# Kernel optimization log

Hardware: AMD Instinct MI355X
Metric: run time of the kernel (lower is better)

The kernel has to match this reference:

```python
import jax, jax.numpy as jnp
import numpy as np

# ---- problem sizes ----
N_CELLS = 128
V_PER = 64            # vertices per cell
F_PER = 124           # faces per cell (2V-4 for closed sphere-like mesh)
N_V = N_CELLS * V_PER # 8192
N_F = N_CELLS * F_PER # 15872

# ---- module hyperparameters (init kwargs) ----
N_ITERS = 5
TIME_STEP = 1e-5
THRESH = 0.3
P_RANGE = (10.0, 200.0)
ST_RANGE = (0.002, 0.02)
TARGET_VOL = 1.0
BULK = 2500.0
UF_ITERS = 8          # label-propagation rounds for union-find


def setup_inputs() -> dict:
    rng = np.random.default_rng(0)
    # cell centers on an 8x4x4 grid, spacing 0.8 so radius-0.5 spheres overlap
    centers = np.stack(np.meshgrid(np.arange(8), np.arange(4), np.arange(4), indexing='ij'), -1)
    centers = centers.reshape(-1, 3).astype(np.float32) * 0.8
    d = rng.normal(size=(N_CELLS, V_PER, 3)).astype(np.float32)
    d /= (np.linalg.norm(d, axis=-1, keepdims=True) + 1e-9)
    verts = (centers[:, None, :] + 0.5 * d).reshape(N_V, 3).astype(np.float32)
    local = rng.integers(0, V_PER, size=(N_CELLS, F_PER, 3))
    faces = (local + np.arange(N_CELLS)[:, None, None] * V_PER).reshape(N_F, 3).astype(np.int32)
    face_cell_index = np.repeat(np.arange(N_CELLS), F_PER).astype(np.int32)
    cell_face_list = np.arange(N_F, dtype=np.int32).reshape(N_CELLS, F_PER)
    vertex_cell = np.repeat(np.arange(N_CELLS), V_PER).astype(np.int32)
    vc = verts.reshape(N_CELLS, V_PER, 3)
    bounding_boxes = np.concatenate([vc.min(1), vc.max(1)], axis=-1).astype(np.float32)
    return {
        'vertices': jnp.asarray(verts),
        'bounding_boxes': jnp.asarray(bounding_boxes),
        'normalized_pressure': jnp.float32(0.5),
        'normalized_surface_tension': jnp.float32(0.5),
        'faces': jnp.asarray(faces),
        'face_cell_index': jnp.asarray(face_cell_index),
        'cell_face_list': jnp.asarray(cell_face_list),
        'vertex_cell': jnp.asarray(vertex_cell),
    }


def _union_find(contact):
    # min-label propagation + pointer jumping; components here are tiny clusters
    def body(_, labels):
        nm = jnp.min(jnp.where(contact, labels[None, :], N_V), axis=1)
        labels = jnp.minimum(labels, nm)
        return labels[labels]
    return jax.lax.fori_loop(0, UF_ITERS, body, jnp.arange(N_V, dtype=jnp.int32))


def _group_mean(x, labels):
    s = jax.ops.segment_sum(x, labels, num_segments=N_V)
    c = jax.ops.segment_sum(jnp.ones((x.shape[0],), x.dtype), labels, num_segments=N_V)
    return (s / jnp.maximum(c, 1.0)[:, None])[labels]


def _energy(verts, faces, cell_face_list, surface_tension, target_vol):
    # surface-tension energy: st * total face area
    v0, v1, v2 = verts[faces[:, 0]], verts[faces[:, 1]], verts[faces[:, 2]]
    n = jnp.cross(v1 - v0, v2 - v0)
    areas = 0.5 * jnp.sqrt(jnp.sum(n * n, -1) + 1e-12)
    e_tension = surface_tension * jnp.sum(areas)
    # pressure/volume energy: K/2 * (V_c - V_target)^2, volume wrt cell centroid
    centroids = verts.reshape(N_CELLS, V_PER, 3).mean(axis=1)  # (C,3)
    fv = faces[cell_face_list]                                  # (C,Fc,3)
    p0 = verts[fv[..., 0]] - centroids[:, None, :]
    p1 = verts[fv[..., 1]] - centroids[:, None, :]
    p2 = verts[fv[..., 2]] - centroids[:, None, :]
    vols = jnp.sum(jnp.einsum('cfi,cfi->cf', p0, jnp.cross(p1, p2)), axis=1) / 6.0
    e_vol = 0.5 * BULK * jnp.sum((vols - target_vol) ** 2)
    return e_tension + e_vol


def _forward(vertices, bounding_boxes, normalized_pressure, normalized_surface_tension,
             faces, cell_face_list, vertex_cell):
    pressure = normalized_pressure * (P_RANGE[1] - P_RANGE[0]) + P_RANGE[0]
    surface_tension = normalized_surface_tension * (ST_RANGE[1] - ST_RANGE[0]) + ST_RANGE[0]
    target_vol = TARGET_VOL * jnp.exp(pressure / BULK)
    # pairwise bbox intersection over cells (fixed bboxes, as in the source)
    mins, maxs = bounding_boxes[:, :3], bounding_boxes[:, 3:]
    cell_contact = (jnp.all(mins[:, None] <= maxs[None, :], -1) &
                    jnp.all(mins[None, :] <= maxs[:, None], -1))
    cell_contact = cell_contact & ~jnp.eye(N_CELLS, dtype=bool)
    verts = vertices
    for _ in range(N_ITERS):
        # pairwise vertex distances, gated by cell contact graph
        sq = jnp.sum(verts * verts, -1)
        d2 = sq[:, None] + sq[None, :] - 2.0 * (verts @ verts.T)
        contact = (d2 < THRESH * THRESH) & cell_contact[vertex_cell[:, None], vertex_cell[None, :]]
        labels = _union_find(contact)
        verts = _group_mean(verts, labels)
        forces = -jax.grad(_energy)(verts, faces, cell_face_list, surface_tension, target_vol)
        forces = _group_mean(forces, labels)
        verts = verts + TIME_STEP * forces
    return verts


def reference(vertices, bounding_boxes, normalized_pressure, normalized_surface_tension,
              faces, face_cell_index, cell_face_list, vertex_cell):
    del face_cell_index  # vertex_cell carries the per-vertex cell ids we need
    return _forward(vertices, bounding_boxes, normalized_pressure, normalized_surface_tension,
                    faces, cell_face_list, vertex_cell)
```

## Files before the change

kernel.cpp:

```cpp
#include <hip/hip_runtime.h>

#define NV 8192
#define NC 128
#define VP 64
#define FP 124
#define MAXSLOT 26
#define NSL 7

typedef unsigned long long ull;

__device__ __forceinline__ int findro(const int* parent, int x) {
  int p = parent[x];
  while (p != x) { x = p; p = parent[x]; }
  return x;
}
__device__ __forceinline__ void ghook(int* parent, int a0, int b0) {
  int a = a0, b = b0;
  for (;;) {
    a = findro(parent, a);
    b = findro(parent, b);
    if (a == b) break;
    int hi = a > b ? a : b, lo = a > b ? b : a;
    int old = atomicMin(&parent[hi], lo);
    if (old == hi) { a = lo; b = lo; break; }
    a = old; b = lo;
  }
  int r = a < b ? a : b;
  if (r < a0) atomicMin(&parent[a0], r);
  if (r < b0) atomicMin(&parent[b0], r);
}

__device__ __forceinline__ void recon3(const float* ps1, const float* ps2,
                                       const float* pc, int l,
                                       float& x, float& y, float& z) {
  float cc = fmaxf(pc[l], 1.f);
  x = ps1[3*l+0]/cc + 1e-5f*(ps2[3*l+0]/cc);
  y = ps1[3*l+1]/cc + 1e-5f*(ps2[3*l+1]/cc);
  z = ps1[3*l+2]/cc + 1e-5f*(ps2[3*l+2]/cc);
}

__device__ __forceinline__ int build_adj(const float* bb, int c, int q, int v,
                                         int t, int* s_hcell, ull* s_adjw,
                                         int* s_KH) {
  if (q < 2) {
    int b = q * 64 + v;
    float anx = bb[c*6+0], any_ = bb[c*6+1], anz = bb[c*6+2];
    float axx = bb[c*6+3], axy = bb[c*6+4], axz = bb[c*6+5];
    float bnx = bb[b*6+0], bny = bb[b*6+1], bnz = bb[b*6+2];
    float bxx = bb[b*6+3], bxy = bb[b*6+4], bxz = bb[b*6+5];
    bool ov = (b != c) && (anx <= bxx) && (any_ <= bxy) && (anz <= bxz) &&
              (bnx <= axx) && (bny <= axy) && (bnz <= axz);
    bool mine = ov && (((c + b) & 1) ? (b < c) : (b > c));
    ull w = __ballot(mine);
    if (v == 0) s_adjw[q] = w;
  }
  __syncthreads();
  if (t == 0) {
    int slot = 0;
    for (int wd = 0; wd < 2; ++wd) {
      ull aw = s_adjw[wd];
      while (aw) {
        int bbit = __ffsll((long long)aw) - 1; aw &= aw - 1;
        if (slot < MAXSLOT) s_hcell[slot] = wd * 64 + bbit;
        ++slot;
      }
    }
    *s_KH = slot;
  }
  __syncthreads();
  return *s_KH;
}

__global__ void k_init(int* __restrict__ parent) {
  int i = blockIdx.x * blockDim.x + threadIdx.x;
  if (i < NV) parent[i] = i;
}

__global__ __launch_bounds__(256, 1)
void k_contact(int it, const float* __restrict__ inV, const float* __restrict__ bb,
               const int* __restrict__ labelsF, const float* __restrict__ ps1,
               const float* __restrict__ pc, const float* __restrict__ ps2,
               float* __restrict__ verts, int* __restrict__ llab,
               ull* __restrict__ masks) {
  const float T2 = (float)(0.3 * 0.3);
  const int c = blockIdx.x;
  const int t = threadIdx.x;
  const int q = t >> 6;
  const int v = t & 63;

  __shared__ float s_vx[VP], s_vy[VP], s_vz[VP], s_sq[VP];
  __shared__ int   s_hcell[MAXSLOT];
  __shared__ int   s_KH;
  __shared__ ull   s_adjw[2];
  __shared__ ull   s_Mw[4][VP];

  const int KH = build_adj(bb, c, q, v, t, s_hcell, s_adjw, &s_KH);

  if (t < VP) {
    int i = c*VP + t;
    float x, y, z;
    if (it == 0) { x = inV[3*i+0]; y = inV[3*i+1]; z = inV[3*i+2]; }
    else         { recon3(ps1, ps2, pc, labelsF[i], x, y, z); }
    s_vx[t] = x; s_vy[t] = y; s_vz[t] = z; s_sq[t] = x*x + y*y + z*z;
    verts[3*i+0] = x; verts[3*i+1] = y; verts[3*i+2] = z;
  }
  __syncthreads();

  ull msk[NSL];
  {
    float xs[NSL], ys[NSL], zs[NSL];
#pragma unroll
    for (int s = 0; s < NSL; ++s) {
      msk[s] = 0;
      int slot = q + 4*s;
      if (slot < KH) {
        int jb = s_hcell[slot]*VP;
        if (it == 0) {
          int j = jb + v;
          xs[s] = inV[3*j+0]; ys[s] = inV[3*j+1]; zs[s] = inV[3*j+2];
        } else {
          int lF = labelsF[jb + v];
          recon3(ps1, ps2, pc, lF, xs[s], ys[s], zs[s]);
        }
      }
    }
#pragma unroll
    for (int s = 0; s < NSL; ++s) { int slot = q + 4*s; if (slot < KH) {
      float X = xs[s], Y = ys[s], Z = zs[s];
      float sqj = X*X + Y*Y + Z*Z;
      ull w = 0;
      for (int vv = 0; vv < VP; ++vv) {
        float d2 = s_sq[vv] + sqj - 2.f*(s_vx[vv]*X + s_vy[vv]*Y + s_vz[vv]*Z);
        if (d2 < T2) w |= (1ull << vv);
      }
      msk[s] = w;
      masks[((size_t)c*MAXSLOT + slot)*VP + v] = w;
    } }
  }

  ull M = 1ull << v;
#pragma unroll
  for (int s = 0; s < NSL; ++s) {
    ull any = __ballot(msk[s] != 0);
    if (any) {
#pragma unroll
      for (int k = 0; k < 64; ++k) {
        ull ck = __shfl(msk[s], k);
        if ((ck >> v) & 1) M |= ck;
      }
    }
  }
  s_Mw[q][v] = M;
  __syncthreads();
  M = s_Mw[0][v] | s_Mw[1][v] | s_Mw[2][v] | s_Mw[3][v];
#pragma unroll
  for (int k = 0; k < 64; ++k) {
    ull rk = __shfl(M, k);
    if ((M >> k) & 1) M |= rk;
  }
  if (q == 0) llab[c*VP + v] = c*VP + (__ffsll((long long)M) - 1);
}

__global__ __launch_bounds__(256, 1)
void k_hook(const float* __restrict__ bb, const int* __restrict__ llab,
            const ull* __restrict__ masks, int* __restrict__ parent) {
  const int c = blockIdx.x;
  const int t = threadIdx.x;
  const int q = t >> 6;
  const int v = t & 63;

  __shared__ int s_hcell[MAXSLOT];
  __shared__ int s_KH;
  __shared__ ull s_adjw[2];

  const int KH = build_adj(bb, c, q, v, t, s_hcell, s_adjw, &s_KH);

#pragma unroll
  for (int s = 0; s < NSL; ++s) { int slot = q + 4*s; if (slot < KH) {
    int jb = s_hcell[slot]*VP;
    ull w = masks[((size_t)c*MAXSLOT + slot)*VP + v];
    int L = -1, Lb = -1;
    if (w) {
      L  = llab[c*VP + (__ffsll((long long)w) - 1)];
      Lb = llab[jb + v];
    }
    ull act = __ballot(w != 0);
    while (act) {
      int lead = __ffsll((long long)act) - 1;
      int Ll  = __shfl(L,  lead);
      int Lbl = __shfl(Lb, lead);
      ull grp = __ballot(L == Ll && Lb == Lbl && w != 0) & act;
      if (v == lead) ghook(parent, Ll, Lbl);
      act &= ~grp;
    }
  } }
}

__global__ __launch_bounds__(64, 1)
void k_find(const int* __restrict__ parent, const int* __restrict__ llab,
            int* __restrict__ labelsF, const float* __restrict__ verts,
            float* __restrict__ cs1, float* __restrict__ cc1,
            float* __restrict__ zs1, float* __restrict__ zc,
            float* __restrict__ zs2) {
  const int c = blockIdx.x, t = threadIdx.x;
  __shared__ int   s_lab[VP];
  __shared__ float s_vx[VP], s_vy[VP], s_vz[VP];
  int i = c*VP + t;
  int l = findro(parent, llab[i]);
  s_lab[t] = l;
  labelsF[i] = l;
  s_vx[t] = verts[3*i+0]; s_vy[t] = verts[3*i+1]; s_vz[t] = verts[3*i+2];
  for (int idx = t; idx < VP*3; idx += VP) {
    zs1[c*VP*3 + idx] = 0.f;
    zs2[c*VP*3 + idx] = 0.f;
  }
  zc[i] = 0.f;
  __syncthreads();
  {
    bool leader = true;
    for (int s = 0; s < t; ++s) if (s_lab[s] == l) { leader = false; break; }
    if (leader) {
      float sx = 0.f, sy = 0.f, sz = 0.f, cn = 0.f;
      for (int s = t; s < VP; ++s)
        if (s_lab[s] == l) { sx += s_vx[s]; sy += s_vy[s]; sz += s_vz[s]; cn += 1.f; }
      atomicAdd(&cs1[3*l+0], sx);
      atomicAdd(&cs1[3*l+1], sy);
      atomicAdd(&cs1[3*l+2], sz);
      atomicAdd(&cc1[l], cn);
    }
  }
}

__global__ __launch_bounds__(128, 1)
void k_forces(const int* __restrict__ labelsF, const int* __restrict__ faces,
              const int* __restrict__ cfl, const float* __restrict__ pP,
              const float* __restrict__ pS,
              const float* __restrict__ cs1, const float* __restrict__ cc1,
              float* __restrict__ cs2, int* __restrict__ parent) {
  const int c = blockIdx.x, t = threadIdx.x;
  __shared__ float s_vx[VP], s_vy[VP], s_vz[VP];
  __shared__ float s_gx[VP], s_gy[VP], s_gz[VP];
  __shared__ float s_fx[VP], s_fy[VP], s_fz[VP];
  __shared__ int   s_lab[VP];
  __shared__ float s_cx, s_cy, s_cz, s_vol, s_csx, s_csy, s_csz;

  if (t < VP) {
    int i = c*VP + t;
    int l = labelsF[i];
    s_lab[t] = l;
    float cc = fmaxf(cc1[l], 1.f);
    s_vx[t] = cs1[3*l+0] / cc;
    s_vy[t] = cs1[3*l+1] / cc;
    s_vz[t] = cs1[3*l+2] / cc;
    s_gx[t] = 0.f; s_gy[t] = 0.f; s_gz[t] = 0.f;
    parent[i] = i;
  }
  if (t == 0) { s_vol = 0.f; s_csx = 0.f; s_csy = 0.f; s_csz = 0.f; }
  __syncthreads();
  if (t < VP) {
    float sx = s_vx[t], sy = s_vy[t], sz = s_vz[t];
#pragma unroll
    for (int o = 32; o; o >>= 1) { sx += __shfl_xor(sx, o); sy += __shfl_xor(sy, o); sz += __shfl_xor(sz, o); }
    if (t == 0) { s_cx = sx*(1.f/VP); s_cy = sy*(1.f/VP); s_cz = sz*(1.f/VP); }
  }
  __syncthreads();
  float cx = s_cx, cy = s_cy, cz = s_cz;
  bool act = (t < FP);
  int ia = 0, ib = 0, ic = 0;
  float p0x=0,p0y=0,p0z=0,p1x=0,p1y=0,p1z=0,p2x=0,p2y=0,p2z=0;
  float q0x=0,q0y=0,q0z=0;
  if (act) {
    int f = cfl[c*FP + t];
    ia = faces[3*f+0] - c*VP; ib = faces[3*f+1] - c*VP; ic = faces[3*f+2] - c*VP;
    p0x = s_vx[ia]-cx; p0y = s_vy[ia]-cy; p0z = s_vz[ia]-cz;
    p1x = s_vx[ib]-cx; p1y = s_vy[ib]-cy; p1z = s_vz[ib]-cz;
    p2x = s_vx[ic]-cx; p2y = s_vy[ic]-cy; p2z = s_vz[ic]-cz;
    q0x = p1y*p2z - p1z*p2y;
    q0y = p1z*p2x - p1x*p2z;
    q0z = p1x*p2y - p1y*p2x;
    float term = p0x*q0x + p0y*q0y + p0z*q0z;
    atomicAdd(&s_vol, term);
  }
  __syncthreads();
  float press = pP[0]*190.f + 10.f;
  float st    = pS[0]*0.018f + 0.002f;
  float tv    = expf(press / 2500.f);
  float vol   = s_vol / 6.f;
  float coeff = 2500.f * (vol - tv);
  if (act) {
    float q1x = p2y*p0z - p2z*p0y;
    float q1y = p2z*p0x - p2x*p0z;
    float q1z = p2x*p0y - p2y*p0x;
    float q2x = p0y*p1z - p0z*p1y;
    float q2y = p0z*p1x - p0x*p1z;
    float q2z = p0x*p1y - p0y*p1x;
    float e1x = p1x-p0x, e1y = p1y-p0y, e1z = p1z-p0z;
    float e2x = p2x-p0x, e2y = p2y-p0y, e2z = p2z-p0z;
    float nx = e1y*e2z - e1z*e2y;
    float ny = e1z*e2x - e1x*e2z;
    float nz = e1x*e2y - e1y*e2x;
    float S  = nx*nx + ny*ny + nz*nz + 1e-12f;
    float wt = st / (2.f * sqrtf(S));
    float dx = e1x-e2x, dy = e1y-e2y, dz = e1z-e2z;
    float g0x = wt*(dy*nz - dz*ny), g0y = wt*(dz*nx - dx*nz), g0z = wt*(dx*ny - dy*nx);
    float g1x = wt*(e2y*nz - e2z*ny), g1y = wt*(e2z*nx - e2x*nz), g1z = wt*(e2x*ny - e2y*nx);
    float g2x = wt*(ny*e1z - nz*e1y), g2y = wt*(nz*e1x - nx*e1z), g2z = wt*(nx*e1y - ny*e1x);
    float k = coeff / 6.f;
    atomicAdd(&s_gx[ia], g0x + k*q0x); atomicAdd(&s_gy[ia], g0y + k*q0y); atomicAdd(&s_gz[ia], g0z + k*q0z);
    atomicAdd(&s_gx[ib], g1x + k*q1x); atomicAdd(&s_gy[ib], g1y + k*q1y); atomicAdd(&s_gz[ib], g1z + k*q1z);
    atomicAdd(&s_gx[ic], g2x + k*q2x); atomicAdd(&s_gy[ic], g2y + k*q2y); atomicAdd(&s_gz[ic], g2z + k*q2z);
    atomicAdd(&s_csx, q0x+q1x+q2x);
    atomicAdd(&s_csy, q0y+q1y+q2y);
    atomicAdd(&s_csz, q0z+q1z+q2z);
  }
  __syncthreads();
  if (t < VP) {
    float corr = coeff / 384.f;
    s_fx[t] = -(s_gx[t] - corr*s_csx);
    s_fy[t] = -(s_gy[t] - corr*s_csy);
    s_fz[t] = -(s_gz[t] - corr*s_csz);
  }
  __syncthreads();
  if (t < VP) {
    int l = s_lab[t];
    bool leader = true;
    for (int s = 0; s < t; ++s) if (s_lab[s] == l) { leader = false; break; }
    if (leader) {
      float sx = 0.f, sy = 0.f, sz = 0.f;
      for (int s = t; s < VP; ++s)
        if (s_lab[s] == l) { sx += s_fx[s]; sy += s_fy[s]; sz += s_fz[s]; }
      atomicAdd(&cs2[3*l+0], sx);
      atomicAdd(&cs2[3*l+1], sy);
      atomicAdd(&cs2[3*l+2], sz);
    }
  }
}

__global__ __launch_bounds__(64, 1)
void k_out(const int* __restrict__ labelsF, const float* __restrict__ cs1,
           const float* __restrict__ cc1, const float* __restrict__ cs2,
           float* __restrict__ out) {
  const int c = blockIdx.x, t = threadIdx.x;
  int i = c*VP + t;
  int l = labelsF[i];
  float cc = fmaxf(cc1[l], 1.f);
  out[3*i+0] = cs1[3*l+0]/cc + 1e-5f*(cs2[3*l+0]/cc);
  out[3*i+1] = cs1[3*l+1]/cc + 1e-5f*(cs2[3*l+1]/cc);
  out[3*i+2] = cs1[3*l+2]/cc + 1e-5f*(cs2[3*l+2]/cc);
}

extern "C" void kernel_launch(void* const* d_in, const int* in_sizes, int n_in,
                              void* d_out, int out_size, void* d_ws, size_t ws_size,
                              hipStream_t stream) {
  const float* inV   = (const float*)d_in[0];
  const float* bb    = (const float*)d_in[1];
  const float* pP    = (const float*)d_in[2];
  const float* pS    = (const float*)d_in[3];
  const int*   faces = (const int*)d_in[4];
  const int*   cfl   = (const int*)d_in[6];

  char* w = (char*)d_ws;
  int*   parent  = (int*)w;   w += NV*sizeof(int);
  int*   labelsF = (int*)w;   w += NV*sizeof(int);
  int*   llab    = (int*)w;   w += NV*sizeof(int);
  float* verts   = (float*)w; w += NV*3*sizeof(float);
  float* zbase   = (float*)w;
  float* sumsA   = (float*)w; w += 2*NV*3*sizeof(float);
  float* countsA = (float*)w; w += 2*NV*sizeof(float);
  float* sumsB   = (float*)w; w += 2*NV*3*sizeof(float);
  ull*   masks   = (ull*)w;   w += (size_t)NC*MAXSLOT*VP*sizeof(ull);

  hipMemsetAsync(zbase, 0, (2*NV*3 + 2*NV + 2*NV*3)*sizeof(float), stream);
  k_init<<<NV/256, 256, 0, stream>>>(parent);

  for (int it = 0; it < 5; ++it) {
    const int p = it & 1;
    float* cs1 = sumsA + p*(NV*3);
    float* cc1 = countsA + p*NV;
    float* cs2 = sumsB + p*(NV*3);
    float* ps1 = sumsA + (p^1)*(NV*3);
    float* pc  = countsA + (p^1)*NV;
    float* ps2 = sumsB + (p^1)*(NV*3);

    k_contact<<<NC, 256, 0, stream>>>(it, inV, bb, labelsF, ps1, pc, ps2,
                                      verts, llab, masks);
    k_hook<<<NC, 256, 0, stream>>>(bb, llab, masks, parent);
    k_find<<<NC, 64, 0, stream>>>(parent, llab, labelsF, verts,
                                  cs1, cc1, ps1, pc, ps2);
    k_forces<<<NC, 128, 0, stream>>>(labelsF, faces, cfl, pP, pS,
                                     cs1, cc1, cs2, parent);
  }
  k_out<<<NC, 64, 0, stream>>>(labelsF, sumsA, countsA, sumsB, (float*)d_out);
}
```

Measured before the change: 411.0 us.

## Fuse hook pass into contact kernel, hooking union-find directly from register masks

```diff
diff --git a/kernel.cpp b/kernel.cpp
--- a/kernel.cpp
+++ b/kernel.cpp
@@ -80,8 +80,7 @@
 void k_contact(int it, const float* __restrict__ inV, const float* __restrict__ bb,
                const int* __restrict__ labelsF, const float* __restrict__ ps1,
                const float* __restrict__ pc, const float* __restrict__ ps2,
-               float* __restrict__ verts, int* __restrict__ llab,
-               ull* __restrict__ masks) {
+               float* __restrict__ verts, int* __restrict__ parent) {
   const float T2 = (float)(0.3 * 0.3);
   const int c = blockIdx.x;
   const int t = threadIdx.x;
@@ -91,6 +90,7 @@
   __shared__ float s_vx[VP], s_vy[VP], s_vz[VP], s_sq[VP];
   __shared__ int   s_hcell[MAXSLOT];
   __shared__ int   s_KH;
+  __shared__ int   s_llv[VP];
   __shared__ ull   s_adjw[2];
   __shared__ ull   s_Mw[4][VP];
 
@@ -134,7 +134,6 @@
         if (d2 < T2) w |= (1ull << vv);
       }
       msk[s] = w;
-      masks[((size_t)c*MAXSLOT + slot)*VP + v] = w;
     } }
   }
 
@@ -158,47 +157,37 @@
     ull rk = __shfl(M, k);
     if ((M >> k) & 1) M |= rk;
   }
-  if (q == 0) llab[c*VP + v] = c*VP + (__ffsll((long long)M) - 1);
-}
-
-__global__ __launch_bounds__(256, 1)
-void k_hook(const float* __restrict__ bb, const int* __restrict__ llab,
-            const ull* __restrict__ masks, int* __restrict__ parent) {
-  const int c = blockIdx.x;
-  const int t = threadIdx.x;
-  const int q = t >> 6;
-  const int v = t & 63;
-
-  __shared__ int s_hcell[MAXSLOT];
-  __shared__ int s_KH;
-  __shared__ ull s_adjw[2];
-
-  const int KH = build_adj(bb, c, q, v, t, s_hcell, s_adjw, &s_KH);
+  const int ll = __ffsll((long long)M) - 1;
+  if (q == 0) s_llv[v] = ll;
+  __syncthreads();
+
+  if (q == 0 && ll != v) ghook(parent, c*VP + v, c*VP + ll);
 
 #pragma unroll
   for (int s = 0; s < NSL; ++s) { int slot = q + 4*s; if (slot < KH) {
     int jb = s_hcell[slot]*VP;
-    ull w = masks[((size_t)c*MAXSLOT + slot)*VP + v];
-    int L = -1, Lb = -1;
-    if (w) {
-      L  = llab[c*VP + (__ffsll((long long)w) - 1)];
-      Lb = llab[jb + v];
-    }
+    ull w = msk[s];
+    int L = -1;
+    if (w) L = s_llv[__ffsll((long long)w) - 1];
+    int myj = jb + v;
     ull act = __ballot(w != 0);
     while (act) {
       int lead = __ffsll((long long)act) - 1;
-      int Ll  = __shfl(L,  lead);
-      int Lbl = __shfl(Lb, lead);
-      ull grp = __ballot(L == Ll && Lb == Lbl && w != 0) & act;
-      if (v == lead) ghook(parent, Ll, Lbl);
+      int Ll = __shfl(L,   lead);
+      int jl = __shfl(myj, lead);
+      ull grp = __ballot(L == Ll && w != 0) & act;
+      if ((grp >> v) & 1) {
+        if (v == lead) ghook(parent, c*VP + Ll, myj);
+        else           ghook(parent, myj, jl);
+      }
       act &= ~grp;
     }
   } }
 }
 
 __global__ __launch_bounds__(64, 1)
-void k_find(const int* __restrict__ parent, const int* __restrict__ llab,
-            int* __restrict__ labelsF, const float* __restrict__ verts,
+void k_find(const int* __restrict__ parent, int* __restrict__ labelsF,
+            const float* __restrict__ verts,
             float* __restrict__ cs1, float* __restrict__ cc1,
             float* __restrict__ zs1, float* __restrict__ zc,
             float* __restrict__ zs2) {
@@ -206,7 +195,7 @@
   __shared__ int   s_lab[VP];
   __shared__ float s_vx[VP], s_vy[VP], s_vz[VP];
   int i = c*VP + t;
-  int l = findro(parent, llab[i]);
+  int l = findro(parent, i);
   s_lab[t] = l;
   labelsF[i] = l;
   s_vx[t] = verts[3*i+0]; s_vy[t] = verts[3*i+1]; s_vz[t] = verts[3*i+2];
@@ -362,13 +351,11 @@
   char* w = (char*)d_ws;
   int*   parent  = (int*)w;   w += NV*sizeof(int);
   int*   labelsF = (int*)w;   w += NV*sizeof(int);
-  int*   llab    = (int*)w;   w += NV*sizeof(int);
   float* verts   = (float*)w; w += NV*3*sizeof(float);
   float* zbase   = (float*)w;
   float* sumsA   = (float*)w; w += 2*NV*3*sizeof(float);
   float* countsA = (float*)w; w += 2*NV*sizeof(float);
   float* sumsB   = (float*)w; w += 2*NV*3*sizeof(float);
-  ull*   masks   = (ull*)w;   w += (size_t)NC*MAXSLOT*VP*sizeof(ull);
 
   hipMemsetAsync(zbase, 0, (2*NV*3 + 2*NV + 2*NV*3)*sizeof(float), stream);
   k_init<<<NV/256, 256, 0, stream>>>(parent);
@@ -383,9 +370,8 @@
     float* ps2 = sumsB + (p^1)*(NV*3);
 
     k_contact<<<NC, 256, 0, stream>>>(it, inV, bb, labelsF, ps1, pc, ps2,
-                                      verts, llab, masks);
-    k_hook<<<NC, 256, 0, stream>>>(bb, llab, masks, parent);
-    k_find<<<NC, 64, 0, stream>>>(parent, llab, labelsF, verts,
+                                      verts, parent);
+    k_find<<<NC, 64, 0, stream>>>(parent, labelsF, verts,
                                   cs1, cc1, ps1, pc, ps2);
     k_forces<<<NC, 128, 0, stream>>>(labelsF, faces, cfl, pP, pS,
                                      cs1, cc1, cs2, parent);
```

Measured after the change: 424.5 us. 3.3% more time.

## Pack cluster sums into float4 and widen contact/hook blocks to 8 waves

Applied to the files above, without the earlier changes.

```diff
diff --git a/kernel.cpp b/kernel.cpp
--- a/kernel.cpp
+++ b/kernel.cpp
@@ -5,7 +5,8 @@
 #define VP 64
 #define FP 124
 #define MAXSLOT 26
-#define NSL 7
+#define NW 8
+#define NSL 4
 
 typedef unsigned long long ull;
 
@@ -28,15 +29,6 @@
   int r = a < b ? a : b;
   if (r < a0) atomicMin(&parent[a0], r);
   if (r < b0) atomicMin(&parent[b0], r);
-}
-
-__device__ __forceinline__ void recon3(const float* ps1, const float* ps2,
-                                       const float* pc, int l,
-                                       float& x, float& y, float& z) {
-  float cc = fmaxf(pc[l], 1.f);
-  x = ps1[3*l+0]/cc + 1e-5f*(ps2[3*l+0]/cc);
-  y = ps1[3*l+1]/cc + 1e-5f*(ps2[3*l+1]/cc);
-  z = ps1[3*l+2]/cc + 1e-5f*(ps2[3*l+2]/cc);
 }
 
 __device__ __forceinline__ int build_adj(const float* bb, int c, int q, int v,
@@ -76,11 +68,11 @@
   if (i < NV) parent[i] = i;
 }
 
-__global__ __launch_bounds__(256, 1)
+__global__ __launch_bounds__(512, 1)
 void k_contact(int it, const float* __restrict__ inV, const float* __restrict__ bb,
-               const int* __restrict__ labelsF, const float* __restrict__ ps1,
-               const float* __restrict__ pc, const float* __restrict__ ps2,
-               float* __restrict__ verts, int* __restrict__ llab,
+               const int* __restrict__ labelsF, const float4* __restrict__ ps1,
+               const float4* __restrict__ ps2,
+               float4* __restrict__ verts4, int* __restrict__ llab,
                ull* __restrict__ masks) {
   const float T2 = (float)(0.3 * 0.3);
   const int c = blockIdx.x;
@@ -92,7 +84,7 @@
   __shared__ int   s_hcell[MAXSLOT];
   __shared__ int   s_KH;
   __shared__ ull   s_adjw[2];
-  __shared__ ull   s_Mw[4][VP];
+  __shared__ ull   s_Mw[NW][VP];
 
   const int KH = build_adj(bb, c, q, v, t, s_hcell, s_adjw, &s_KH);
 
@@ -100,9 +92,16 @@
     int i = c*VP + t;
     float x, y, z;
     if (it == 0) { x = inV[3*i+0]; y = inV[3*i+1]; z = inV[3*i+2]; }
-    else         { recon3(ps1, ps2, pc, labelsF[i], x, y, z); }
+    else {
+      int l = labelsF[i];
+      float4 a = ps1[l], b = ps2[l];
+      float cc = fmaxf(a.w, 1.f);
+      x = a.x/cc + 1e-5f*(b.x/cc);
+      y = a.y/cc + 1e-5f*(b.y/cc);
+      z = a.z/cc + 1e-5f*(b.z/cc);
+    }
     s_vx[t] = x; s_vy[t] = y; s_vz[t] = z; s_sq[t] = x*x + y*y + z*z;
-    verts[3*i+0] = x; verts[3*i+1] = y; verts[3*i+2] = z;
+    verts4[i] = make_float4(x, y, z, 0.f);
   }
   __syncthreads();
 
@@ -112,20 +111,24 @@
 #pragma unroll
     for (int s = 0; s < NSL; ++s) {
       msk[s] = 0;
-      int slot = q + 4*s;
+      int slot = q + NW*s;
       if (slot < KH) {
         int jb = s_hcell[slot]*VP;
         if (it == 0) {
           int j = jb + v;
           xs[s] = inV[3*j+0]; ys[s] = inV[3*j+1]; zs[s] = inV[3*j+2];
         } else {
-          int lF = labelsF[jb + v];
-          recon3(ps1, ps2, pc, lF, xs[s], ys[s], zs[s]);
+          int l = labelsF[jb + v];
+          float4 a = ps1[l], b = ps2[l];
+          float cc = fmaxf(a.w, 1.f);
+          xs[s] = a.x/cc + 1e-5f*(b.x/cc);
+          ys[s] = a.y/cc + 1e-5f*(b.y/cc);
+          zs[s] = a.z/cc + 1e-5f*(b.z/cc);
         }
       }
     }
 #pragma unroll
-    for (int s = 0; s < NSL; ++s) { int slot = q + 4*s; if (slot < KH) {
+    for (int s = 0; s < NSL; ++s) { int slot = q + NW*s; if (slot < KH) {
       float X = xs[s], Y = ys[s], Z = zs[s];
       float sqj = X*X + Y*Y + Z*Z;
       ull w = 0;
@@ -152,7 +155,8 @@
   }
   s_Mw[q][v] = M;
   __syncthreads();
-  M = s_Mw[0][v] | s_Mw[1][v] | s_Mw[2][v] | s_Mw[3][v];
+  M = s_Mw[0][v] | s_Mw[1][v] | s_Mw[2][v] | s_Mw[3][v] |
+      s_Mw[4][v] | s_Mw[5][v] | s_Mw[6][v] | s_Mw[7][v];
 #pragma unroll
   for (int k = 0; k < 64; ++k) {
     ull rk = __shfl(M, k);
@@ -161,7 +165,7 @@
   if (q == 0) llab[c*VP + v] = c*VP + (__ffsll((long long)M) - 1);
 }
 
-__global__ __launch_bounds__(256, 1)
+__global__ __launch_bounds__(512, 1)
 void k_hook(const float* __restrict__ bb, const int* __restrict__ llab,
             const ull* __restrict__ masks, int* __restrict__ parent) {
   const int c = blockIdx.x;
@@ -176,7 +180,7 @@
   const int KH = build_adj(bb, c, q, v, t, s_hcell, s_adjw, &s_KH);
 
 #pragma unroll
-  for (int s = 0; s < NSL; ++s) { int slot = q + 4*s; if (slot < KH) {
+  for (int s = 0; s < NSL; ++s) { int slot = q + NW*s; if (slot < KH) {
     int jb = s_hcell[slot]*VP;
     ull w = masks[((size_t)c*MAXSLOT + slot)*VP + v];
     int L = -1, Lb = -1;
@@ -198,10 +202,9 @@
 
 __global__ __launch_bounds__(64, 1)
 void k_find(const int* __restrict__ parent, const int* __restrict__ llab,
-            int* __restrict__ labelsF, const float* __restrict__ verts,
-            float* __restrict__ cs1, float* __restrict__ cc1,
-            float* __restrict__ zs1, float* __restrict__ zc,
-            float* __restrict__ zs2) {
+            int* __restrict__ labelsF, const float4* __restrict__ verts4,
+            float4* __restrict__ cs1, float4* __restrict__ zs1,
+            float4* __restrict__ zs2) {
   const int c = blockIdx.x, t = threadIdx.x;
   __shared__ int   s_lab[VP];
   __shared__ float s_vx[VP], s_vy[VP], s_vz[VP];
@@ -209,12 +212,10 @@
   int l = findro(parent, llab[i]);
   s_lab[t] = l;
   labelsF[i] = l;
-  s_vx[t] = verts[3*i+0]; s_vy[t] = verts[3*i+1]; s_vz[t] = verts[3*i+2];
-  for (int idx = t; idx < VP*3; idx += VP) {
-    zs1[c*VP*3 + idx] = 0.f;
-    zs2[c*VP*3 + idx] = 0.f;
-  }
-  zc[i] = 0.f;
+  float4 vv = verts4[i];
+  s_vx[t] = vv.x; s_vy[t] = vv.y; s_vz[t] = vv.z;
+  zs1[i] = make_float4(0.f, 0.f, 0.f, 0.f);
+  zs2[i] = make_float4(0.f, 0.f, 0.f, 0.f);
   __syncthreads();
   {
     bool leader = true;
@@ -223,10 +224,10 @@
       float sx = 0.f, sy = 0.f, sz = 0.f, cn = 0.f;
       for (int s = t; s < VP; ++s)
         if (s_lab[s] == l) { sx += s_vx[s]; sy += s_vy[s]; sz += s_vz[s]; cn += 1.f; }
-      atomicAdd(&cs1[3*l+0], sx);
-      atomicAdd(&cs1[3*l+1], sy);
-      atomicAdd(&cs1[3*l+2], sz);
-      atomicAdd(&cc1[l], cn);
+      atomicAdd(&cs1[l].x, sx);
+      atomicAdd(&cs1[l].y, sy);
+      atomicAdd(&cs1[l].z, sz);
+      atomicAdd(&cs1[l].w, cn);
     }
   }
 }
@@ -235,8 +236,8 @@
 void k_forces(const int* __restrict__ labelsF, const int* __restrict__ faces,
               const int* __restrict__ cfl, const float* __restrict__ pP,
               const float* __restrict__ pS,
-              const float* __restrict__ cs1, const float* __restrict__ cc1,
-              float* __restrict__ cs2, int* __restrict__ parent) {
+              const float4* __restrict__ cs1, float4* __restrict__ cs2,
+              int* __restrict__ parent) {
   const int c = blockIdx.x, t = threadIdx.x;
   __shared__ float s_vx[VP], s_vy[VP], s_vz[VP];
   __shared__ float s_gx[VP], s_gy[VP], s_gz[VP];
@@ -248,10 +249,11 @@
     int i = c*VP + t;
     int l = labelsF[i];
     s_lab[t] = l;
-    float cc = fmaxf(cc1[l], 1.f);
-    s_vx[t] = cs1[3*l+0] / cc;
-    s_vy[t] = cs1[3*l+1] / cc;
-    s_vz[t] = cs1[3*l+2] / cc;
+    float4 a = cs1[l];
+    float cc = fmaxf(a.w, 1.f);
+    s_vx[t] = a.x / cc;
+    s_vy[t] = a.y / cc;
+    s_vz[t] = a.z / cc;
     s_gx[t] = 0.f; s_gy[t] = 0.f; s_gz[t] = 0.f;
     parent[i] = i;
   }
@@ -329,24 +331,24 @@
       float sx = 0.f, sy = 0.f, sz = 0.f;
       for (int s = t; s < VP; ++s)
         if (s_lab[s] == l) { sx += s_fx[s]; sy += s_fy[s]; sz += s_fz[s]; }
-      atomicAdd(&cs2[3*l+0], sx);
-      atomicAdd(&cs2[3*l+1], sy);
-      atomicAdd(&cs2[3*l+2], sz);
+      atomicAdd(&cs2[l].x, sx);
+      atomicAdd(&cs2[l].y, sy);
+      atomicAdd(&cs2[l].z, sz);
     }
   }
 }
 
 __global__ __launch_bounds__(64, 1)
-void k_out(const int* __restrict__ labelsF, const float* __restrict__ cs1,
-           const float* __restrict__ cc1, const float* __restrict__ cs2,
-           float* __restrict__ out) {
+void k_out(const int* __restrict__ labelsF, const float4* __restrict__ cs1,
+           const float4* __restrict__ cs2, float* __restrict__ out) {
   const int c = blockIdx.x, t = threadIdx.x;
   int i = c*VP + t;
   int l = labelsF[i];
-  float cc = fmaxf(cc1[l], 1.f);
-  out[3*i+0] = cs1[3*l+0]/cc + 1e-5f*(cs2[3*l+0]/cc);
-  out[3*i+1] = cs1[3*l+1]/cc + 1e-5f*(cs2[3*l+1]/cc);
-  out[3*i+2] = cs1[3*l+2]/cc + 1e-5f*(cs2[3*l+2]/cc);
+  float4 a = cs1[l], b = cs2[l];
+  float cc = fmaxf(a.w, 1.f);
+  out[3*i+0] = a.x/cc + 1e-5f*(b.x/cc);
+  out[3*i+1] = a.y/cc + 1e-5f*(b.y/cc);
+  out[3*i+2] = a.z/cc + 1e-5f*(b.z/cc);
 }
 
 extern "C" void kernel_launch(void* const* d_in, const int* in_sizes, int n_in,
@@ -360,35 +362,32 @@
   const int*   cfl   = (const int*)d_in[6];
 
   char* w = (char*)d_ws;
-  int*   parent  = (int*)w;   w += NV*sizeof(int);
-  int*   labelsF = (int*)w;   w += NV*sizeof(int);
-  int*   llab    = (int*)w;   w += NV*sizeof(int);
-  float* verts   = (float*)w; w += NV*3*sizeof(float);
-  float* zbase   = (float*)w;
-  float* sumsA   = (float*)w; w += 2*NV*3*sizeof(float);
-  float* countsA = (float*)w; w += 2*NV*sizeof(float);
-  float* sumsB   = (float*)w; w += 2*NV*3*sizeof(float);
-  ull*   masks   = (ull*)w;   w += (size_t)NC*MAXSLOT*VP*sizeof(ull);
-
-  hipMemsetAsync(zbase, 0, (2*NV*3 + 2*NV + 2*NV*3)*sizeof(float), stream);
+  int*    parent  = (int*)w;    w += NV*sizeof(int);
+  int*    labelsF = (int*)w;    w += NV*sizeof(int);
+  int*    llab    = (int*)w;    w += NV*sizeof(int);
+  float4* verts4  = (float4*)w; w += NV*sizeof(float4);
+  float4* zbase   = (float4*)w;
+  float4* sumsA   = (float4*)w; w += 2*NV*sizeof(float4);
+  float4* sumsB   = (float4*)w; w += 2*NV*sizeof(float4);
+  ull*    masks   = (ull*)w;    w += (size_t)NC*MAXSLOT*VP*sizeof(ull);
+
+  hipMemsetAsync(zbase, 0, 4*NV*sizeof(float4), stream);
   k_init<<<NV/256, 256, 0, stream>>>(parent);
 
   for (int it = 0; it < 5; ++it) {
     const int p = it & 1;
-    float* cs1 = sumsA + p*(NV*3);
-    float* cc1 = countsA + p*NV;
-    float* cs2 = sumsB + p*(NV*3);
-    float* ps1 = sumsA + (p^1)*(NV*3);
-    float* pc  = countsA + (p^1)*NV;
-    float* ps2 = sumsB + (p^1)*(NV*3);
-
-    k_contact<<<NC, 256, 0, stream>>>(it, inV, bb, labelsF, ps1, pc, ps2,
-                                      verts, llab, masks);
-    k_hook<<<NC, 256, 0, stream>>>(bb, llab, masks, parent);
-    k_find<<<NC, 64, 0, stream>>>(parent, llab, labelsF, verts,
-                                  cs1, cc1, ps1, pc, ps2);
+    float4* cs1 = sumsA + p*NV;
+    float4* cs2 = sumsB + p*NV;
+    float4* ps1 = sumsA + (p^1)*NV;
+    float4* ps2 = sumsB + (p^1)*NV;
+
+    k_contact<<<NC, 512, 0, stream>>>(it, inV, bb, labelsF, ps1, ps2,
+                                      verts4, llab, masks);
+    k_hook<<<NC, 512, 0, stream>>>(bb, llab, masks, parent);
+    k_find<<<NC, 64, 0, stream>>>(parent, llab, labelsF, verts4,
+                                  cs1, ps1, ps2);
     k_forces<<<NC, 128, 0, stream>>>(labelsF, faces, cfl, pP, pS,
-                                     cs1, cc1, cs2, parent);
-  }
-  k_out<<<NC, 64, 0, stream>>>(labelsF, sumsA, countsA, sumsB, (float*)d_out);
-}
+                                     cs1, cs2, parent);
+  }
+  k_out<<<NC, 64, 0, stream>>>(labelsF, sumsA, sumsB, (float*)d_out);
+}
```

New measurement: 371.6 us. -9.6%, faster.
